# Kernel optimization log

Hardware: AMD Instinct MI355X
Metric: run time of the kernel (lower is better)

Reference implementation:

```python
import jax, jax.numpy as jnp
import numpy as np

LN_EPS = 1e-5
NEG_SLOPE = 0.01  # torch LeakyReLU default


def layernorm(x, w, b):
    m = jnp.mean(x, axis=-1, keepdims=True)
    v = jnp.mean((x - m) ** 2, axis=-1, keepdims=True)
    return (x - m) * jax.lax.rsqrt(v + LN_EPS) * w + b


def setup_inputs() -> dict:
    key = jax.random.key(0)
    ks = jax.random.split(key, 12)
    B, T, C, E = 16, 1024, 768, 2
    d = C
    s = 0.02
    inp = {
        "x": jax.random.normal(ks[0], (B, T, C), jnp.float32),
        "ln1_w": jnp.ones((C,), jnp.float32),
        "ln1_b": jnp.zeros((C,), jnp.float32),
        "wqkv": jax.random.normal(ks[1], (C, 3 * C), jnp.float32) * s,
        "bqkv": jnp.zeros((3 * C,), jnp.float32),
        "wproj": jax.random.normal(ks[2], (C, C), jnp.float32) * s,
        "bproj": jnp.zeros((C,), jnp.float32),
        "ln2_w": jnp.ones((C,), jnp.float32),
        "ln2_b": jnp.zeros((C,), jnp.float32),
        "wg": jax.random.normal(ks[3], (C, E), jnp.float32) * s,
        # Experts module uses torch.randn (std 1); we scale down for numerics
        "w1": jax.random.normal(ks[4], (E, d, 4 * d), jnp.float32) * s,
        "w2": jax.random.normal(ks[5], (E, 4 * d, 4 * d), jnp.float32) * s,
        "w3": jax.random.normal(ks[6], (E, 4 * d, d), jnp.float32) * s,
        "n_head": 12,
    }
    return inp


def block_forward(x, ln1_w, ln1_b, wqkv, bqkv, wproj, bproj,
                  ln2_w, ln2_b, wg, w1, w2, w3, n_head):
    B, T, C = x.shape
    H = n_head
    hd = C // H
    E = wg.shape[-1]

    # ---- causal self-attention + residual ----
    h = layernorm(x, ln1_w, ln1_b)
    qkv = h @ wqkv + bqkv                      # [B,T,3C]
    q, k, v = jnp.split(qkv, 3, axis=-1)
    q = q.reshape(B, T, H, hd).transpose(0, 2, 1, 3)  # bhtd
    k = k.reshape(B, T, H, hd).transpose(0, 2, 1, 3)
    v = v.reshape(B, T, H, hd).transpose(0, 2, 1, 3)
    scores = jnp.einsum('bhqd,bhkd->bhqk', q, k) / jnp.sqrt(jnp.float32(hd))
    causal = jnp.tril(jnp.ones((T, T), bool))
    scores = jnp.where(causal, scores, jnp.finfo(scores.dtype).min)
    attn = jax.nn.softmax(scores, axis=-1)
    y = jnp.einsum('bhqk,bhkd->bhqd', attn, v)
    y = y.transpose(0, 2, 1, 3).reshape(B, T, C)
    x = x + (y @ wproj + bproj)

    # ---- MoE (top-2 gating, capacity dispatch) + residual ----
    h2 = layernorm(x, ln2_w, ln2_b)
    capacity = (T * 2) // E                    # capacity_factor = 1.0, top-2
    raw_gates = jax.nn.softmax(h2 @ wg, axis=-1)   # [B,T,E]

    idx1 = jnp.argmax(raw_gates, axis=-1)
    mask1 = jax.nn.one_hot(idx1, E, dtype=raw_gates.dtype)
    gate1 = jnp.sum(raw_gates * mask1, axis=-1)    # [B,T]
    gates2 = raw_gates * (1.0 - mask1)
    idx2 = jnp.argmax(gates2, axis=-1)
    mask2 = jax.nn.one_hot(idx2, E, dtype=raw_gates.dtype)
    gate2 = jnp.sum(raw_gates * mask2, axis=-1)
    denom = gate1 + gate2 + 1e-9
    gate1, gate2 = gate1 / denom, gate2 / denom

    # aux load-balancing loss (before capacity truncation)
    density = jnp.mean(mask1, axis=1)              # [B,E]
    density_proxy = jnp.mean(raw_gates, axis=1)    # [B,E]
    aux_loss = jnp.mean(density * density_proxy) * (E * E)

    # positions within each expert buffer (exclusive cumsum over tokens)
    pos1 = jnp.cumsum(mask1, axis=1) - mask1       # [B,T,E]
    mask1 = mask1 * (pos1 < capacity)
    mask1_count = jnp.sum(mask1, axis=1, keepdims=True)
    pos2 = (jnp.cumsum(mask2, axis=1) - mask2) + mask1_count
    mask2 = mask2 * (pos2 < capacity)

    oh1 = jax.nn.one_hot(pos1.astype(jnp.int32), capacity, dtype=raw_gates.dtype)
    oh2 = jax.nn.one_hot(pos2.astype(jnp.int32), capacity, dtype=raw_gates.dtype)
    combine = (gate1[..., None] * mask1)[..., None] * oh1 \
            + (gate2[..., None] * mask2)[..., None] * oh2   # [B,T,E,C]
    dispatch = (combine > 0).astype(h2.dtype)

    # dispatch -> per-expert batches
    expert_in = jnp.einsum('bnd,bnec->ebcd', h2, dispatch)   # [E,B,Cap,d]
    Bc = B * capacity
    ei = expert_in.reshape(E, Bc, C)
    lrelu = lambda z: jnp.where(z >= 0, z, NEG_SLOPE * z)
    hh = lrelu(jnp.einsum('end,edh->enh', ei, w1))
    hh = lrelu(jnp.einsum('end,edh->enh', hh, w2))
    eo = jnp.einsum('end,edh->enh', hh, w3).reshape(E, B, capacity, C)
    moe_out = jnp.einsum('ebcd,bnec->bnd', eo, combine)

    x = x + moe_out
    return x, aux_loss


def reference(x, ln1_w, ln1_b, wqkv, bqkv, wproj, bproj,
              ln2_w, ln2_b, wg, w1, w2, w3, n_head):
    return block_forward(x, ln1_w, ln1_b, wqkv, bqkv, wproj, bproj,
                         ln2_w, ln2_b, wg, w1, w2, w3, n_head)
```

## Files before the change

kernel.cpp:

```cpp
#include <hip/hip_runtime.h>
#include <cstdint>
#include <cstddef>

constexpr int B_  = 16;
constexpr int T_  = 1024;
constexpr int C_  = 768;
constexpr int H_  = 12;
constexpr int HD_ = 64;
constexpr int BT_ = B_ * T_;
constexpr int C3_ = 3 * C_;
constexpr int QK2_ = 2 * C_;
constexpr int FF_ = 4 * C_;
constexpr int MCH_ = 8192;

typedef __bf16 bf16x8 __attribute__((ext_vector_type(8)));
typedef float  floatx4 __attribute__((ext_vector_type(4)));
typedef unsigned short u16x8 __attribute__((ext_vector_type(8)));

__device__ inline float bf2f(unsigned short u) {
  union { unsigned int i; float f; } x; x.i = ((unsigned int)u) << 16; return x.f;
}
__device__ inline unsigned short f2bf(float f) {
  union { float f; unsigned int i; } x; x.f = f;
  unsigned int u = x.i;
  u += 0x7fffu + ((u >> 16) & 1u);
  return (unsigned short)(u >> 16);
}

#define GLOAD_LDS16(gp, lp)                                              \
  __builtin_amdgcn_global_load_lds(                                      \
      (__attribute__((address_space(1))) void*)(gp),                     \
      (__attribute__((address_space(3))) void*)(lp), 16, 0, 0)

__launch_bounds__(256)
__global__ void ln_kernel(const float* __restrict__ x, const float* __restrict__ w,
                          const float* __restrict__ b, unsigned short* __restrict__ out) {
  int row = blockIdx.x;
  int tid = threadIdx.x;
  const float* xr = x + (size_t)row * C_;
  float v0 = xr[tid], v1 = xr[tid + 256], v2 = xr[tid + 512];
  float s  = v0 + v1 + v2;
  float ss = v0 * v0 + v1 * v1 + v2 * v2;
#pragma unroll
  for (int off = 32; off > 0; off >>= 1) {
    s  += __shfl_down(s, off, 64);
    ss += __shfl_down(ss, off, 64);
  }
  __shared__ float red[8];
  int wid = tid >> 6;
  if ((tid & 63) == 0) { red[wid] = s; red[4 + wid] = ss; }
  __syncthreads();
  float st  = red[0] + red[1] + red[2] + red[3];
  float sst = red[4] + red[5] + red[6] + red[7];
  float mean = st * (1.0f / C_);
  float var  = sst * (1.0f / C_) - mean * mean;
  float rstd = rsqrtf(var + 1e-5f);
  unsigned short* orow = out + (size_t)row * C_;
  orow[tid]       = f2bf((v0 - mean) * rstd * w[tid]       + b[tid]);
  orow[tid + 256] = f2bf((v1 - mean) * rstd * w[tid + 256] + b[tid + 256]);
  orow[tid + 512] = f2bf((v2 - mean) * rstd * w[tid + 512] + b[tid + 512]);
}

struct CtJobs {
  const float* in[8];
  unsigned short* out[8];
  int K[8], N[8], tX[8];
  int t0[9];
};

__launch_bounds__(256)
__global__ void convT_batch(CtJobs J) {
  __shared__ float t[32][33];
  int bid = blockIdx.x;
  int ji = 0;
#pragma unroll
  for (int i = 0; i < 7; ++i) ji += (bid >= J.t0[i + 1]) ? 1 : 0;
  const float* in = J.in[ji];
  unsigned short* out = J.out[ji];
  const int K = J.K[ji], N = J.N[ji];
  const int lt = bid - J.t0[ji];
  const int bx = lt % J.tX[ji], by = lt / J.tX[ji];
  const int n0 = bx * 32, k0 = by * 32;
  const int tx = threadIdx.x & 31, ty = threadIdx.x >> 5;
#pragma unroll
  for (int r = 0; r < 32; r += 8)
    t[r + ty][tx] = in[(size_t)(k0 + r + ty) * N + n0 + tx];
  __syncthreads();
#pragma unroll
  for (int r = 0; r < 32; r += 8)
    out[(size_t)(n0 + r + ty) * K + k0 + tx] = f2bf(t[tx][r + ty]);
}

template <int ACT, bool BIAS, bool RES, bool COMBINE, bool OUTBF16,
          bool VSPLIT = false, bool ZB = false>
__launch_bounds__(256)
__global__ void gemm_bf16(const unsigned short* __restrict__ A,
                          const unsigned short* __restrict__ Bt,
                          const float* __restrict__ bias,
                          const float* __restrict__ Rres,
                          const float* __restrict__ gates2, int eidx,
                          void* __restrict__ Cout,
                          unsigned short* __restrict__ vtout,
                          int M, int N, int K,
                          size_t zsA, size_t zsB) {
  __shared__ __attribute__((aligned(16))) unsigned short Als[8192];
  __shared__ __attribute__((aligned(16))) unsigned short Bls[8192];
  const int tid  = threadIdx.x;
  const int wave = tid >> 6, lane = tid & 63;
  const int wr = wave >> 1, wc = wave & 1;

  if (ZB) {
    A  += (size_t)blockIdx.z * zsA;
    Bt += (size_t)blockIdx.z * zsB;
    eidx = (int)blockIdx.z;
  }

  int bx = blockIdx.x, by = blockIdx.y;
  {
    const int nbx = gridDim.x;
    const int nwg = nbx * gridDim.y;
    if ((nwg & 7) == 0) {
      const int bid = by * nbx + bx;
      const int swz = (bid & 7) * (nwg >> 3) + (bid >> 3);
      by = swz / nbx; bx = swz - by * nbx;
    }
  }
  const int m0 = by * 128, n0 = bx * 128;

  const int srow = wave * 32 + (lane >> 3);
  const int skg  = (lane & 7) ^ ((lane >> 3) & 7);
  const unsigned short* Ap = A  + (size_t)(m0 + srow) * K + skg * 8;
  const unsigned short* Bp = Bt + (size_t)(n0 + srow) * K + skg * 8;
  unsigned short* AlsW = Als + wave * 2048;
  unsigned short* BlsW = Bls + wave * 2048;

  floatx4 acc[4][4];
#pragma unroll
  for (int i = 0; i < 4; ++i)
#pragma unroll
    for (int j = 0; j < 4; ++j) acc[i][j] = floatx4{0.f, 0.f, 0.f, 0.f};

  const int q  = lane >> 4;
  const int ml = lane & 15;
  const int rsw = ml & 7;

  for (int k0 = 0; k0 < K; k0 += 64) {
    __syncthreads();
#pragma unroll
    for (int i = 0; i < 4; ++i) {
      GLOAD_LDS16(Ap + (size_t)(i * 8) * K + k0, AlsW + i * 512);
      GLOAD_LDS16(Bp + (size_t)(i * 8) * K + k0, BlsW + i * 512);
    }
    __syncthreads();
#pragma unroll
    for (int ks = 0; ks < 2; ++ks) {
      const int p = (ks * 4 + q) ^ rsw;
      bf16x8 af[4], bfg[4];
#pragma unroll
      for (int i = 0; i < 4; ++i) {
        int ar = wr * 64 + i * 16 + ml;
        af[i]  = *(const bf16x8*)&Als[(ar * 8 + p) * 8];
        int br = wc * 64 + i * 16 + ml;
        bfg[i] = *(const bf16x8*)&Bls[(br * 8 + p) * 8];
      }
#pragma unroll
      for (int i = 0; i < 4; ++i)
#pragma unroll
        for (int j = 0; j < 4; ++j)
          acc[i][j] = __builtin_amdgcn_mfma_f32_16x16x32_bf16(af[i], bfg[j], acc[i][j], 0, 0, 0);
    }
  }

  const int rbase = q * 4;
#pragma unroll
  for (int i = 0; i < 4; ++i) {
    int row = m0 + wr * 64 + i * 16 + rbase;
#pragma unroll
    for (int j = 0; j < 4; ++j) {
      int col = n0 + wc * 64 + j * 16 + ml;
      float bcol = BIAS ? bias[col] : 0.f;
#pragma unroll
      for (int r = 0; r < 4; ++r) {
        float v = acc[i][j][r];
        if (BIAS) v += bcol;
        if (ACT == 1) v = (v >= 0.f) ? v : 0.01f * v;
        if (RES) v += Rres[(size_t)(row + r) * N + col];
        if (COMBINE) {
          float g = gates2[2 * (row + r) + eidx];
          float* op = (float*)Cout + (size_t)(row + r) * N + col;
          if (ZB) atomicAdd(op, g * v);
          else    *op += g * v;
        } else if (VSPLIT) {
          if (col < QK2_) {
            ((unsigned short*)Cout)[(size_t)(row + r) * QK2_ + col] = f2bf(v);
          } else {
            vtout[(size_t)(col - QK2_) * BT_ + row + r] = f2bf(v);
          }
        } else if (OUTBF16) {
          ((unsigned short*)Cout)[(size_t)(row + r) * N + col] = f2bf(v);
        } else {
          ((float*)Cout)[(size_t)(row + r) * N + col] = v;
        }
      }
    }
  }
}

#define GB256_BAR()   asm volatile("s_barrier" ::: "memory")
#define GB256_LGKM0() asm volatile("s_waitcnt lgkmcnt(0)" ::: "memory")

template <int ACT, bool BIAS>
__launch_bounds__(512, 2)
__global__ void gemm256(const unsigned short* __restrict__ A,
                        const unsigned short* __restrict__ Bt,
                        const float* __restrict__ bias,
                        unsigned short* __restrict__ Cout,
                        int M, int N, int K,
                        size_t zsA, size_t zsB, size_t zsC) {
  __shared__ __attribute__((aligned(16))) unsigned short L[65536];
  const int tid = threadIdx.x;
  const int w = tid >> 6, l = tid & 63;
  const int wr = w >> 2, wc = w & 3;
  const int ml = l & 15, q = l >> 4;
  const int m0 = blockIdx.y * 256, n0 = blockIdx.x * 256;

  A    += (size_t)blockIdx.z * zsA;
  Bt   += (size_t)blockIdx.z * zsB;
  Cout += (size_t)blockIdx.z * zsC;

  const int srow = l >> 2;
  const int sg   = ((l & 3) ^ ((l >> 3) & 3)) * 8;
  const unsigned short* Ast = A  + (size_t)(m0 + srow) * K + sg;
  const unsigned short* Bst = Bt + (size_t)(n0 + srow) * K + sg;
  const int ldsw = w * 1024;

#define STG(cb, mat, ks, srcp, kk)                                           \
  do {                                                                       \
    const unsigned short* _s = (srcp) + (size_t)(w * 32) * K + (kk) + (ks) * 32; \
    unsigned short* _d = L + (cb) * 32768 + (mat) * 16384 + (ks) * 8192 + ldsw;  \
    GLOAD_LDS16(_s, _d);                                                     \
    GLOAD_LDS16(_s + (size_t)16 * K, _d + 512);                              \
  } while (0)

  const int dphys = (q ^ ((ml >> 1) & 3)) * 8;
  const int aoff = (wr * 128 + ml) * 32 + dphys;
  const int boff = (wc * 64 + ml) * 32 + dphys;

  floatx4 acc[8][4];
#pragma unroll
  for (int m = 0; m < 8; ++m)
#pragma unroll
    for (int n = 0; n < 4; ++n) acc[m][n] = floatx4{0.f, 0.f, 0.f, 0.f};

  const int NT = K >> 6;

  STG(0, 0, 0, Ast, 0);  STG(0, 1, 0, Bst, 0);
  STG(0, 0, 1, Ast, 0);  STG(0, 1, 1, Bst, 0);
  STG(1, 0, 0, Ast, 64); STG(1, 1, 0, Bst, 64);
  asm volatile("s_waitcnt vmcnt(0)" ::: "memory");
  GB256_BAR();

  for (int j = 0; j < NT; ++j) {
    const int c = j & 1, nx = c ^ 1;
    const int kk1 = (j + 1) << 6, kk2 = (j + 2) << 6;
    const bool st1 = (j + 1 < NT), st2 = (j + 2 < NT);
    bf16x8 bA[4], bB[4];

#define LOAD_A(KS, MH)                                                       \
  _Pragma("unroll")                                                          \
  for (int mq = 0; mq < 4; ++mq)                                             \
    bA[mq] = *(const bf16x8*)&L[c * 32768 + (KS) * 8192 + aoff + ((MH) * 4 + mq) * 512];
#define LOAD_B(KS)                                                           \
  _Pragma("unroll")                                                          \
  for (int n = 0; n < 4; ++n)                                                \
    bB[n] = *(const bf16x8*)&L[c * 32768 + 16384 + (KS) * 8192 + boff + n * 512];
#define MFMA16(MH)                                                           \
  __builtin_amdgcn_s_setprio(1);                                             \
  _Pragma("unroll")                                                          \
  for (int mq = 0; mq < 4; ++mq)                                             \
    _Pragma("unroll")                                                        \
    for (int n = 0; n < 4; ++n)                                              \
      acc[(MH) * 4 + mq][n] = __builtin_amdgcn_mfma_f32_16x16x32_bf16(       \
          bA[mq], bB[n], acc[(MH) * 4 + mq][n], 0, 0, 0);                    \
  __builtin_amdgcn_s_setprio(0);

    LOAD_B(0); LOAD_A(0, 0);
    if (st1) STG(nx, 0, 1, Ast, kk1);
    GB256_BAR(); GB256_LGKM0();
    MFMA16(0);
    GB256_BAR();

    LOAD_A(0, 1);
    if (st1) STG(nx, 1, 1, Bst, kk1);
    GB256_BAR(); GB256_LGKM0();
    MFMA16(1);
    GB256_BAR();

    LOAD_B(1); LOAD_A(1, 0);
    if (st2) STG(c, 0, 0, Ast, kk2);
    GB256_BAR(); GB256_LGKM0();
    MFMA16(0);
    GB256_BAR();

    LOAD_A(1, 1);
    if (st2) STG(c, 1, 0, Bst, kk2);
    GB256_BAR(); GB256_LGKM0();
    MFMA16(1);
    if (st2)      asm volatile("s_waitcnt vmcnt(4)" ::: "memory");
    else if (st1) asm volatile("s_waitcnt vmcnt(0)" ::: "memory");
    GB256_BAR();
#undef LOAD_A
#undef LOAD_B
#undef MFMA16
  }

#pragma unroll
  for (int m = 0; m < 8; ++m) {
    const int row = m0 + wr * 128 + m * 16 + q * 4;
#pragma unroll
    for (int n = 0; n < 4; ++n) {
      const int col = n0 + wc * 64 + n * 16 + ml;
      const float bcol = BIAS ? bias[col] : 0.f;
#pragma unroll
      for (int r = 0; r < 4; ++r) {
        float v = acc[m][n][r];
        if (BIAS) v += bcol;
        if (ACT == 1) v = (v >= 0.f) ? v : 0.01f * v;
        Cout[(size_t)(row + r) * N + col] = f2bf(v);
      }
    }
  }
#undef STG
}

__launch_bounds__(256)
__global__ void attn_kernel(const unsigned short* __restrict__ qk,
                            const unsigned short* __restrict__ vT,
                            unsigned short* __restrict__ y) {
  __shared__ __attribute__((aligned(16))) unsigned short Qls[64 * 64];
  __shared__ __attribute__((aligned(16))) unsigned short K2[2][64 * 64];
  __shared__ __attribute__((aligned(16))) unsigned short V2[2][64 * 64];
  __shared__ __attribute__((aligned(16))) unsigned short Pls[4 * 16 * 72];

  const int tid  = threadIdx.x;
  const int wave = tid >> 6, lane = tid & 63;
  const int quad = lane >> 4, n = lane & 15;
  const int q0 = blockIdx.x * 64;
  const int bh = blockIdx.y;
  const int b = bh / H_, h = bh % H_;
  const size_t qbase = (size_t)b * T_ * QK2_ + (size_t)h * HD_;
  const size_t vbase = (size_t)h * HD_ * BT_ + (size_t)b * T_;

  const int r8 = lane >> 3;
  const int g  = (lane & 7) ^ r8;

#pragma unroll
  for (int i = 0; i < 2; ++i) {
    int row = wave * 16 + i * 8 + r8;
    GLOAD_LDS16(qk + qbase + (size_t)(q0 + row) * QK2_ + g * 8,
                Qls + wave * 1024 + i * 512);
  }

#define STAGE_KV(bf, k0)                                                      \
  do {                                                                        \
    _Pragma("unroll")                                                         \
    for (int i = 0; i < 2; ++i) {                                             \
      int row = wave * 16 + i * 8 + r8;                                       \
      GLOAD_LDS16(qk + qbase + (size_t)((k0) + row) * QK2_ + C_ + g * 8,      \
                  K2[bf] + wave * 1024 + i * 512);                            \
      GLOAD_LDS16(vT + vbase + (size_t)row * BT_ + (k0) + g * 8,              \
                  V2[bf] + wave * 1024 + i * 512);                            \
    }                                                                         \
  } while (0)

  STAGE_KV(0, 0);

  floatx4 O[4];
#pragma unroll
  for (int ct = 0; ct < 4; ++ct) O[ct] = floatx4{0.f, 0.f, 0.f, 0.f};
  float mrow[4] = {-1e30f, -1e30f, -1e30f, -1e30f};
  float lrow[4] = {0.f, 0.f, 0.f, 0.f};

  const int nkt = blockIdx.x + 1;
  unsigned short* Pw = Pls + wave * (16 * 72);

  for (int kt = 0; kt < nkt; ++kt) {
    const int cur = kt & 1;
    __syncthreads();
    if (kt + 1 < nkt) STAGE_KV(cur ^ 1, (kt + 1) << 6);

    floatx4 sacc[4];
#pragma unroll
    for (int ct = 0; ct < 4; ++ct) sacc[ct] = floatx4{0.f, 0.f, 0.f, 0.f};
#pragma unroll
    for (int ks = 0; ks < 2; ++ks) {
      const int ga = (ks * 4 + quad) ^ (n & 7);
      bf16x8 aq = *(const bf16x8*)&Qls[((wave * 16 + n) * 8 + ga) * 8];
#pragma unroll
      for (int ct = 0; ct < 4; ++ct) {
        bf16x8 kb = *(const bf16x8*)&K2[cur][((ct * 16 + n) * 8 + ga) * 8];
        sacc[ct] = __builtin_amdgcn_mfma_f32_16x16x32_bf16(aq, kb, sacc[ct], 0, 0, 0);
      }
    }

    float p[4][4];
#pragma unroll
    for (int ct = 0; ct < 4; ++ct)
#pragma unroll
      for (int r = 0; r < 4; ++r) p[ct][r] = sacc[ct][r] * 0.125f;
    if (kt == nkt - 1) {
      const int kgb = (kt << 6) + n, qgb = q0 + wave * 16 + quad * 4;
#pragma unroll
      for (int ct = 0; ct < 4; ++ct)
#pragma unroll
        for (int r = 0; r < 4; ++r)
          if (kgb + ct * 16 > qgb + r) p[ct][r] = -1e30f;
    }
#pragma unroll
    for (int r = 0; r < 4; ++r) {
      float tm = fmaxf(fmaxf(p[0][r], p[1][r]), fmaxf(p[2][r], p[3][r]));
      tm = fmaxf(tm, __shfl_xor(tm, 1, 64));
      tm = fmaxf(tm, __shfl_xor(tm, 2, 64));
      tm = fmaxf(tm, __shfl_xor(tm, 4, 64));
      tm = fmaxf(tm, __shfl_xor(tm, 8, 64));
      float mn = fmaxf(mrow[r], tm);
      float alpha = __expf(mrow[r] - mn);
      mrow[r] = mn;
      float ps = 0.f;
#pragma unroll
      for (int ct = 0; ct < 4; ++ct) {
        float pe = __expf(p[ct][r] - mn);
        p[ct][r] = pe;
        ps += pe;
      }
      ps += __shfl_xor(ps, 1, 64);
      ps += __shfl_xor(ps, 2, 64);
      ps += __shfl_xor(ps, 4, 64);
      ps += __shfl_xor(ps, 8, 64);
      lrow[r] = lrow[r] * alpha + ps;
      O[0][r] *= alpha; O[1][r] *= alpha; O[2][r] *= alpha; O[3][r] *= alpha;
    }

#pragma unroll
    for (int ct = 0; ct < 4; ++ct)
#pragma unroll
      for (int r = 0; r < 4; ++r)
        Pw[(quad * 4 + r) * 72 + ct * 16 + n] = f2bf(p[ct][r]);

#pragma unroll
    for (int ks = 0; ks < 2; ++ks) {
      bf16x8 pa = *(const bf16x8*)&Pw[n * 72 + (ks * 4 + quad) * 8];
      const int gv = (ks * 4 + quad) ^ (n & 7);
#pragma unroll
      for (int ct = 0; ct < 4; ++ct) {
        bf16x8 vb = *(const bf16x8*)&V2[cur][((ct * 16 + n) * 8 + gv) * 8];
        O[ct] = __builtin_amdgcn_mfma_f32_16x16x32_bf16(pa, vb, O[ct], 0, 0, 0);
      }
    }
  }

#pragma unroll
  for (int r = 0; r < 4; ++r) {
    float inv = 1.0f / lrow[r];
    int row = q0 + wave * 16 + quad * 4 + r;
    unsigned short* dst = y + ((size_t)b * T_ + row) * C_ + h * HD_;
#pragma unroll
    for (int ct = 0; ct < 4; ++ct)
      dst[ct * 16 + n] = f2bf(O[ct][r] * inv);
  }
#undef STAGE_KV
}

__launch_bounds__(256)
__global__ void gate_kernel(const unsigned short* __restrict__ h2,
                            const float* __restrict__ wg,
                            float* __restrict__ gates) {
  int wave = threadIdx.x >> 6, lane = threadIdx.x & 63;
  int t = blockIdx.x * 4 + wave;
  const unsigned short* hr = h2 + (size_t)t * C_;
  float a0 = 0.0f, a1 = 0.0f;
#pragma unroll
  for (int i = 0; i < 12; ++i) {
    int d = lane + 64 * i;
    float hv = bf2f(hr[d]);
    a0 += hv * wg[2 * d];
    a1 += hv * wg[2 * d + 1];
  }
#pragma unroll
  for (int off = 32; off > 0; off >>= 1) {
    a0 += __shfl_down(a0, off, 64);
    a1 += __shfl_down(a1, off, 64);
  }
  if (lane == 0) {
    float m  = fmaxf(a0, a1);
    float e0 = __expf(a0 - m), e1 = __expf(a1 - m);
    float invs = 1.0f / (e0 + e1);
    float p0 = e0 * invs, p1 = e1 * invs;
    const float gnorm = 1.0f / (1.0f + 1e-9f);
    gates[2 * t]     = p0 * gnorm;
    gates[2 * t + 1] = p1 * gnorm;
  }
}

__launch_bounds__(1024)
__global__ void moe_stats_kernel(const float* __restrict__ gates,
                                 float* __restrict__ out_aux) {
  int wave = threadIdx.x >> 6, lane = threadIdx.x & 63;
  float c0 = 0.f, sp0 = 0.f, sp1 = 0.f;
#pragma unroll
  for (int j = 0; j < 16; ++j) {
    int t = wave * T_ + lane + 64 * j;
    float p0 = gates[2 * t], p1 = gates[2 * t + 1];
    c0  += (p1 > p0) ? 0.f : 1.f;
    sp0 += p0;
    sp1 += p1;
  }
#pragma unroll
  for (int off = 32; off > 0; off >>= 1) {
    c0  += __shfl_down(c0, off, 64);
    sp0 += __shfl_down(sp0, off, 64);
    sp1 += __shfl_down(sp1, off, 64);
  }
  __shared__ float red[16][3];
  if (lane == 0) { red[wave][0] = c0; red[wave][1] = sp0; red[wave][2] = sp1; }
  __syncthreads();
  if (threadIdx.x == 0) {
    float s = 0.f;
    for (int b = 0; b < B_; ++b) {
      float cc0 = red[b][0];
      float d0 = cc0 * (1.f / T_), d1 = (T_ - cc0) * (1.f / T_);
      float px0 = red[b][1] * (1.f / T_), px1 = red[b][2] * (1.f / T_);
      s += d0 * px0 + d1 * px1;
    }
    out_aux[0] = s * (4.f / 32.f);
  }
}

extern "C" void kernel_launch(void* const* d_in, const int* in_sizes, int n_in,
                              void* d_out, int out_size, void* d_ws, size_t ws_size,
                              hipStream_t stream) {
  const float* x     = (const float*)d_in[0];
  const float* ln1_w = (const float*)d_in[1];
  const float* ln1_b = (const float*)d_in[2];
  const float* wqkv  = (const float*)d_in[3];
  const float* bqkv  = (const float*)d_in[4];
  const float* wproj = (const float*)d_in[5];
  const float* bproj = (const float*)d_in[6];
  const float* ln2_w = (const float*)d_in[7];
  const float* ln2_b = (const float*)d_in[8];
  const float* wg    = (const float*)d_in[9];
  const float* w1    = (const float*)d_in[10];
  const float* w2    = (const float*)d_in[11];
  const float* w3    = (const float*)d_in[12];
  float* out = (float*)d_out;

  unsigned short* wsu   = (unsigned short*)d_ws;
  unsigned short* wqkvT = wsu;
  unsigned short* wprojT= wqkvT + (size_t)C3_ * C_;
  unsigned short* w1T   = wprojT + (size_t)C_ * C_;
  unsigned short* w2T   = w1T + (size_t)2 * FF_ * C_;
  unsigned short* w3T   = w2T + (size_t)2 * FF_ * FF_;
  unsigned short* hb    = w3T + (size_t)2 * C_ * FF_;
  unsigned short* region= hb + (size_t)BT_ * C_;
  unsigned short* qkb   = region;
  unsigned short* vTb   = region + (size_t)BT_ * QK2_;
  unsigned short* yb    = region + (size_t)BT_ * 3 * C_;

  const size_t regionElems = (size_t)BT_ * 4 * C_;
  const size_t bigElems    = (size_t)4 * MCH_ * FF_;
  const size_t baseElems   = (size_t)(region - wsu);
  const bool   big = ws_size >= (baseElems + bigElems + 65536) * sizeof(unsigned short);

  float* gates = (float*)(region + (big ? bigElems : regionElems));

  {
    CtJobs J;
    int idx = 0, acc = 0;
    auto add = [&](const float* in, unsigned short* outp, int K, int N) {
      J.in[idx] = in; J.out[idx] = outp; J.K[idx] = K; J.N[idx] = N;
      J.tX[idx] = N / 32; J.t0[idx] = acc;
      acc += (N / 32) * (K / 32);
      ++idx;
    };
    add(wqkv, wqkvT, C_, C3_);
    add(wproj, wprojT, C_, C_);
    for (int e = 0; e < 2; ++e) {
      add(w1 + (size_t)e * C_ * FF_, w1T + (size_t)e * FF_ * C_, C_, FF_);
      add(w2 + (size_t)e * FF_ * FF_, w2T + (size_t)e * FF_ * FF_, FF_, FF_);
      add(w3 + (size_t)e * FF_ * C_, w3T + (size_t)e * C_ * FF_, FF_, C_);
    }
    J.t0[8] = acc;
    convT_batch<<<acc, 256, 0, stream>>>(J);
  }

  ln_kernel<<<BT_, 256, 0, stream>>>(x, ln1_w, ln1_b, hb);
  gemm_bf16<0, true, false, false, true, true><<<dim3(C3_ / 128, BT_ / 128), 256, 0, stream>>>(
      hb, wqkvT, bqkv, nullptr, nullptr, 0, qkb, vTb, BT_, C3_, C_, 0, 0);
  attn_kernel<<<dim3(T_ / 64, B_ * H_), 256, 0, stream>>>(qkb, vTb, yb);
  gemm_bf16<0, true, true, false, false><<<dim3(C_ / 128, BT_ / 128), 256, 0, stream>>>(
      yb, wprojT, bproj, x, nullptr, 0, out, nullptr, BT_, C_, C_, 0, 0);

  ln_kernel<<<BT_, 256, 0, stream>>>(out, ln2_w, ln2_b, hb);
  gate_kernel<<<BT_ / 4, 256, 0, stream>>>(hb, wg, gates);
  moe_stats_kernel<<<1, 1024, 0, stream>>>(gates, out + (size_t)BT_ * C_);

  if (big) {
    unsigned short* hh1b = region;
    unsigned short* hh2b = region + (size_t)2 * MCH_ * FF_;
    for (int c = 0; c < BT_ / MCH_; ++c) {
      const unsigned short* a = hb + (size_t)c * MCH_ * C_;
      gemm256<1, false><<<dim3(FF_ / 256, MCH_ / 256, 2), 512, 0, stream>>>(
          a, w1T, nullptr, hh1b, MCH_, FF_, C_,
          0, (size_t)FF_ * C_, (size_t)MCH_ * FF_);
      gemm256<1, false><<<dim3(FF_ / 256, MCH_ / 256, 2), 512, 0, stream>>>(
          hh1b, w2T, nullptr, hh2b, MCH_, FF_, FF_,
          (size_t)MCH_ * FF_, (size_t)FF_ * FF_, (size_t)MCH_ * FF_);
      gemm_bf16<0, false, false, true, false, false, true>
          <<<dim3(C_ / 128, MCH_ / 128, 2), 256, 0, stream>>>(
          hh2b, w3T, nullptr, nullptr,
          gates + (size_t)2 * c * MCH_, 0, out + (size_t)c * MCH_ * C_, nullptr,
          MCH_, C_, FF_, (size_t)MCH_ * FF_, (size_t)C_ * FF_);
    }
  } else {
    unsigned short* hh1 = region;
    unsigned short* hh2 = region + (size_t)MCH_ * FF_;
    for (int e = 0; e < 2; ++e) {
      for (int c = 0; c < BT_ / MCH_; ++c) {
        const unsigned short* a = hb + (size_t)c * MCH_ * C_;
        gemm_bf16<1, false, false, false, true><<<dim3(FF_ / 128, MCH_ / 128), 256, 0, stream>>>(
            a, w1T + (size_t)e * FF_ * C_, nullptr, nullptr, nullptr, 0, hh1, nullptr,
            MCH_, FF_, C_, 0, 0);
        gemm_bf16<1, false, false, false, true><<<dim3(FF_ / 128, MCH_ / 128), 256, 0, stream>>>(
            hh1, w2T + (size_t)e * FF_ * FF_, nullptr, nullptr, nullptr, 0, hh2, nullptr,
            MCH_, FF_, FF_, 0, 0);
        gemm_bf16<0, false, false, true, false><<<dim3(C_ / 128, MCH_ / 128), 256, 0, stream>>>(
            hh2, w3T + (size_t)e * C_ * FF_, nullptr, nullptr,
            gates + (size_t)2 * c * MCH_, e, out + (size_t)c * MCH_ * C_, nullptr,
            MCH_, C_, FF_, 0, 0);
      }
    }
  }
}
```

Before: 1.624 ms.

## Simplify gemm256 pipeline to one barrier per k-step and use it for w3 combine

After: 1.624 ms. No clear change (+0.0%).

```diff
diff --git a/kernel.cpp b/kernel.cpp
--- a/kernel.cpp
+++ b/kernel.cpp
@@ -207,14 +207,15 @@
 }
 
 #define GB256_BAR()   asm volatile("s_barrier" ::: "memory")
-#define GB256_LGKM0() asm volatile("s_waitcnt lgkmcnt(0)" ::: "memory")
-
-template <int ACT, bool BIAS>
+
+template <int ACT, bool BIAS, bool COMBINE = false>
 __launch_bounds__(512, 2)
 __global__ void gemm256(const unsigned short* __restrict__ A,
                         const unsigned short* __restrict__ Bt,
                         const float* __restrict__ bias,
                         unsigned short* __restrict__ Cout,
+                        const float* __restrict__ gates2,
+                        float* __restrict__ outF,
                         int M, int N, int K,
                         size_t zsA, size_t zsB, size_t zsC) {
   __shared__ __attribute__((aligned(16))) unsigned short L[65536];
@@ -223,10 +224,11 @@
   const int wr = w >> 2, wc = w & 3;
   const int ml = l & 15, q = l >> 4;
   const int m0 = blockIdx.y * 256, n0 = blockIdx.x * 256;
-
-  A    += (size_t)blockIdx.z * zsA;
-  Bt   += (size_t)blockIdx.z * zsB;
-  Cout += (size_t)blockIdx.z * zsC;
+  const int z  = (int)blockIdx.z;
+
+  A  += (size_t)z * zsA;
+  Bt += (size_t)z * zsB;
+  if (!COMBINE) Cout += (size_t)z * zsC;
 
   const int srow = l >> 2;
   const int sg   = ((l & 3) ^ ((l >> 3) & 3)) * 8;
@@ -254,16 +256,15 @@
 
   const int NT = K >> 6;
 
-  STG(0, 0, 0, Ast, 0);  STG(0, 1, 0, Bst, 0);
-  STG(0, 0, 1, Ast, 0);  STG(0, 1, 1, Bst, 0);
-  STG(1, 0, 0, Ast, 64); STG(1, 1, 0, Bst, 64);
+  STG(0, 0, 0, Ast, 0); STG(0, 1, 0, Bst, 0);
+  STG(0, 0, 1, Ast, 0); STG(0, 1, 1, Bst, 0);
   asm volatile("s_waitcnt vmcnt(0)" ::: "memory");
   GB256_BAR();
 
   for (int j = 0; j < NT; ++j) {
     const int c = j & 1, nx = c ^ 1;
-    const int kk1 = (j + 1) << 6, kk2 = (j + 2) << 6;
-    const bool st1 = (j + 1 < NT), st2 = (j + 2 < NT);
+    const int kk1 = (j + 1) << 6;
+    const bool st1 = (j + 1 < NT);
     bf16x8 bA[4], bB[4];
 
 #define LOAD_A(KS, MH)                                                       \
@@ -284,31 +285,20 @@
           bA[mq], bB[n], acc[(MH) * 4 + mq][n], 0, 0, 0);                    \
   __builtin_amdgcn_s_setprio(0);
 
-    LOAD_B(0); LOAD_A(0, 0);
-    if (st1) STG(nx, 0, 1, Ast, kk1);
-    GB256_BAR(); GB256_LGKM0();
-    MFMA16(0);
-    GB256_BAR();
-
-    LOAD_A(0, 1);
-    if (st1) STG(nx, 1, 1, Bst, kk1);
-    GB256_BAR(); GB256_LGKM0();
-    MFMA16(1);
-    GB256_BAR();
-
-    LOAD_B(1); LOAD_A(1, 0);
-    if (st2) STG(c, 0, 0, Ast, kk2);
-    GB256_BAR(); GB256_LGKM0();
-    MFMA16(0);
-    GB256_BAR();
-
-    LOAD_A(1, 1);
-    if (st2) STG(c, 1, 0, Bst, kk2);
-    GB256_BAR(); GB256_LGKM0();
-    MFMA16(1);
-    if (st2)      asm volatile("s_waitcnt vmcnt(4)" ::: "memory");
-    else if (st1) asm volatile("s_waitcnt vmcnt(0)" ::: "memory");
-    GB256_BAR();
+    if (st1) {
+      STG(nx, 0, 0, Ast, kk1); STG(nx, 1, 0, Bst, kk1);
+      STG(nx, 0, 1, Ast, kk1); STG(nx, 1, 1, Bst, kk1);
+    }
+
+    LOAD_B(0); LOAD_A(0, 0); MFMA16(0);
+    LOAD_A(0, 1);            MFMA16(1);
+    LOAD_B(1); LOAD_A(1, 0); MFMA16(0);
+    LOAD_A(1, 1);            MFMA16(1);
+
+    if (st1) {
+      asm volatile("s_waitcnt vmcnt(0)" ::: "memory");
+      GB256_BAR();
+    }
 #undef LOAD_A
 #undef LOAD_B
 #undef MFMA16
@@ -326,7 +316,12 @@
         float v = acc[m][n][r];
         if (BIAS) v += bcol;
         if (ACT == 1) v = (v >= 0.f) ? v : 0.01f * v;
-        Cout[(size_t)(row + r) * N + col] = f2bf(v);
+        if (COMBINE) {
+          float g = gates2[2 * (row + r) + z];
+          atomicAdd(outF + (size_t)(row + r) * N + col, g * v);
+        } else {
+          Cout[(size_t)(row + r) * N + col] = f2bf(v);
+        }
       }
     }
   }
@@ -610,16 +605,16 @@
     for (int c = 0; c < BT_ / MCH_; ++c) {
       const unsigned short* a = hb + (size_t)c * MCH_ * C_;
       gemm256<1, false><<<dim3(FF_ / 256, MCH_ / 256, 2), 512, 0, stream>>>(
-          a, w1T, nullptr, hh1b, MCH_, FF_, C_,
+          a, w1T, nullptr, hh1b, nullptr, nullptr, MCH_, FF_, C_,
           0, (size_t)FF_ * C_, (size_t)MCH_ * FF_);
       gemm256<1, false><<<dim3(FF_ / 256, MCH_ / 256, 2), 512, 0, stream>>>(
-          hh1b, w2T, nullptr, hh2b, MCH_, FF_, FF_,
+          hh1b, w2T, nullptr, hh2b, nullptr, nullptr, MCH_, FF_, FF_,
           (size_t)MCH_ * FF_, (size_t)FF_ * FF_, (size_t)MCH_ * FF_);
-      gemm_bf16<0, false, false, true, false, false, true>
-          <<<dim3(C_ / 128, MCH_ / 128, 2), 256, 0, stream>>>(
+      gemm256<0, false, true><<<dim3(C_ / 256, MCH_ / 256, 2), 512, 0, stream>>>(
           hh2b, w3T, nullptr, nullptr,
-          gates + (size_t)2 * c * MCH_, 0, out + (size_t)c * MCH_ * C_, nullptr,
-          MCH_, C_, FF_, (size_t)MCH_ * FF_, (size_t)C_ * FF_);
+          gates + (size_t)2 * c * MCH_, out + (size_t)c * MCH_ * C_,
+          MCH_, C_, FF_,
+          (size_t)MCH_ * FF_, (size_t)C_ * FF_, 0);
     }
   } else {
     unsigned short* hh1 = region;
```
